# Performance work log

Hardware: AMD Instinct MI355X
Metric: run time of the kernel (lower is better)

## Reference

```python
import jax, jax.numpy as jnp
import numpy as np

TT_IN = (8, 8, 8, 8)
TT_OUT = (8, 8, 8, 8)
TT_RANKS = (1, 32, 32, 32, 1)
BATCH = 4096
N_IN = int(np.prod(TT_IN))     # 4096
N_OUT = int(np.prod(TT_OUT))   # 4096
KERNEL_LEN = int(sum(TT_RANKS[k] * TT_IN[k] * TT_OUT[k] * TT_RANKS[k + 1]
                     for k in range(len(TT_IN))))  # 135168


def setup_inputs() -> dict:
    key = jax.random.key(0)
    kx, kk = jax.random.split(key)
    x = jax.random.normal(kx, (BATCH, N_IN), dtype=jnp.float32)
    # flat packed TT cores (the layer stores all cores in one 1-D weight)
    kernel = 0.02 * jax.random.normal(kk, (KERNEL_LEN,), dtype=jnp.float32)
    bias = jnp.zeros((N_OUT,), dtype=jnp.float32)
    return {"x": x, "kernel": kernel, "bias": bias}


def reference(x, kernel, bias):
    # Faithful translation of TensorTrainDense.call: iterate cores k = d-1 .. 0,
    # slicing the flat kernel from index 0 (matching the original code exactly).
    batch = x.shape[0]
    res = x
    idx = 0
    for k in range(len(TT_IN) - 1, -1, -1):
        m = TT_IN[k] * TT_RANKS[k + 1]   # contraction dim
        n = TT_RANKS[k] * TT_OUT[k]      # output dim of this core
        core = kernel[idx:idx + m * n].reshape(m, n)
        res = res.reshape(-1, m) @ core              # (-1, r_k*out_k)
        res = res.reshape(-1, TT_OUT[k]).T           # (out_k, -1)
        idx += m * n
    res = res.reshape(-1, batch).T                   # (batch, prod(out))
    return res + bias
```

## Files before the change

kernel.cpp:

```cpp
#include <hip/hip_runtime.h>
#include <hip/hip_bf16.h>

typedef unsigned short u16;
typedef __attribute__((ext_vector_type(8))) short  bf16x8;
typedef __attribute__((ext_vector_type(4))) float  fx4;

#define OFF_C0 0
#define OFF_C1 2048
#define OFF_C2 67584
#define OFF_C3 133120

static __device__ __forceinline__ u16 f2bf(float f) {
  union { __hip_bfloat16 h; u16 u; } cv;
  cv.h = __float2bfloat16(f);
  return cv.u;
}
static __device__ __forceinline__ float bf2f(u16 u) {
  union { u16 u; __hip_bfloat16 h; } cv;
  cv.u = u;
  return __bfloat162float(cv.h);
}

__global__ void x_and_w34T(const float* __restrict__ x, u16* __restrict__ xb,
                           const float* __restrict__ ker, float* __restrict__ w34T) {
  if (blockIdx.x < 8192) {
    int t = blockIdx.x * 256 + threadIdx.x;
    const fx4* p = (const fx4*)(x + (size_t)t * 8);
    fx4 v0 = p[0], v1 = p[1];
    u16 tmp[8];
#pragma unroll
    for (int q = 0; q < 4; ++q) tmp[q] = f2bf(v0[q]);
#pragma unroll
    for (int q = 0; q < 4; ++q) tmp[4 + q] = f2bf(v1[q]);
    typedef __attribute__((ext_vector_type(8))) u16 u16x8;
    *(u16x8*)(xb + (size_t)t * 8) = *(const u16x8*)tmp;
  } else {
    int t = (blockIdx.x - 8192) * 256 + threadIdx.x;
    int i34 = t & 63, c = t >> 6;
    int a2 = c >> 6, o3 = (c >> 3) & 7, o4 = c & 7;
    int i3 = i34 >> 3, i4 = i34 & 7;
    float s = 0.f;
#pragma unroll 8
    for (int a3 = 0; a3 < 32; ++a3) {
      float k1 = ker[OFF_C1 + (i3 * 32 + a3) * 256 + a2 * 8 + o3];
      float k0 = ker[OFF_C0 + i4 * 256 + a3 * 8 + o4];
      s += k1 * k0;
    }
    w34T[c * 64 + i34] = s;
  }
}

__global__ void build_w234t2(const float* __restrict__ ker, const float* __restrict__ w34T,
                             u16* __restrict__ w234t) {
  int t = blockIdx.x * 256 + threadIdx.x;
  int i234 = t & 511, g = t >> 9;
  int a1 = g >> 3, o3 = g & 7;
  int i2 = i234 >> 6, i34 = i234 & 63;
  float acc[8][8];
#pragma unroll
  for (int a = 0; a < 8; ++a)
#pragma unroll
    for (int b = 0; b < 8; ++b) acc[a][b] = 0.f;
  for (int a2 = 0; a2 < 32; ++a2) {
    float w[8];
#pragma unroll
    for (int o4 = 0; o4 < 8; ++o4)
      w[o4] = w34T[(a2 * 64 + o3 * 8 + o4) * 64 + i34];
#pragma unroll
    for (int o2 = 0; o2 < 8; ++o2) {
      float c2 = ker[OFF_C2 + (i2 * 32 + a2) * 256 + a1 * 8 + o2];
#pragma unroll
      for (int o4 = 0; o4 < 8; ++o4) acc[o2][o4] += c2 * w[o4];
    }
  }
#pragma unroll
  for (int o2 = 0; o2 < 8; ++o2) {
    int cg = a1 * 64 + o2 * 8 + o3;
#pragma unroll
    for (int o4 = 0; o4 < 8; ++o4)
      w234t[(cg * 8 + o4) * 512 + i234] = f2bf(acc[o2][o4]);
  }
}

__global__ void build_wt2(const float* __restrict__ ker, const u16* __restrict__ w234t,
                          u16* __restrict__ wt) {
  int t = blockIdx.x * 256 + threadIdx.x;
  int i234 = t & 511, j234 = t >> 9;
  float acc[8][8];
#pragma unroll
  for (int a = 0; a < 8; ++a)
#pragma unroll
    for (int b = 0; b < 8; ++b) acc[a][b] = 0.f;
  for (int a1 = 0; a1 < 32; ++a1) {
    float w = bf2f(w234t[(a1 * 512 + j234) * 512 + i234]);
#pragma unroll
    for (int i1 = 0; i1 < 8; ++i1) {
      const float* c3 = ker + OFF_C3 + (i1 * 32 + a1) * 8;
#pragma unroll
      for (int o1 = 0; o1 < 8; ++o1) acc[i1][o1] += c3[o1] * w;
    }
  }
#pragma unroll
  for (int o1 = 0; o1 < 8; ++o1)
#pragma unroll
    for (int i1 = 0; i1 < 8; ++i1)
      wt[(size_t)(o1 * 512 + j234) * 4096 + i1 * 512 + i234] = f2bf(acc[i1][o1]);
}

__device__ __forceinline__ void gld16(const u16* g, u16* l) {
  __builtin_amdgcn_global_load_lds((const __attribute__((address_space(1))) void*)g,
                                   (__attribute__((address_space(3))) void*)l, 16, 0, 0);
}

__global__ __launch_bounds__(256, 2) void gemm_half(const u16* __restrict__ A, const u16* __restrict__ Bt,
                                                    const float* __restrict__ bias, float* __restrict__ C) {
  __shared__ __align__(16) u16 sh[36864];

  const int tid = threadIdx.x;
  const int lane = tid & 63;
  const int wave = tid >> 6;
  const int wm = wave >> 1, wn = wave & 1;
  const int fr = lane & 15, fg = lane >> 4;

  const int bid = blockIdx.x;
  const int wg = (bid & 7) * 64 + (bid >> 3);
  const int bm = (wg >> 4) * 128, bn = (wg & 15) * 256;

  const int lq = lane >> 2, ls = lane & 3;
  size_t agA[2], agB[4];
#pragma unroll
  for (int L = 0; L < 2; ++L) {
    const int row = (wave * 2 + L) * 16 + lq;
    agA[L] = (size_t)(bm + row) * 4096 + ((ls ^ ((row >> 1) & 3)) * 8);
  }
#pragma unroll
  for (int L = 0; L < 4; ++L) {
    const int row = (wave * 4 + L) * 16 + lq;
    agB[L] = (size_t)(bn + row) * 4096 + ((ls ^ ((row >> 1) & 3)) * 8);
  }
  u16* const ldA0 = sh + (wave * 2) * 512;
  u16* const ldB0 = sh + 12288 + (wave * 4) * 512;

  int aoff[4], boff[8];
#pragma unroll
  for (int m = 0; m < 4; ++m) {
    const int R = wm * 64 + m * 16 + fr;
    aoff[m] = R * 32 + ((fg ^ ((R >> 1) & 3)) * 8);
  }
#pragma unroll
  for (int n = 0; n < 8; ++n) {
    const int R = wn * 128 + n * 16 + fr;
    boff[n] = R * 32 + ((fg ^ ((R >> 1) & 3)) * 8);
  }

  fx4 acc[4][8];
#pragma unroll
  for (int m = 0; m < 4; ++m)
#pragma unroll
    for (int n = 0; n < 8; ++n) acc[m][n] = (fx4){0.f, 0.f, 0.f, 0.f};

#define STAGE(buf, t) do { const size_t k_ = (size_t)(((t) & 127) * 32); \
    u16* a_ = ldA0 + (buf) * 4096; u16* b_ = ldB0 + (buf) * 8192; \
    gld16(A + agA[0] + k_, a_); \
    gld16(A + agA[1] + k_, a_ + 512); \
    gld16(Bt + agB[0] + k_, b_); \
    gld16(Bt + agB[1] + k_, b_ + 512); \
    gld16(Bt + agB[2] + k_, b_ + 1024); \
    gld16(Bt + agB[3] + k_, b_ + 1536); } while (0)

  STAGE(0, 0);
  STAGE(1, 1);
  asm volatile("s_waitcnt vmcnt(6)" ::: "memory");
  __builtin_amdgcn_s_barrier();

  int p = 0;
  for (int t = 0; t < 128; ++t) {
    const int ps = p + 2 >= 3 ? p - 1 : p + 2;
    const u16* Ap = sh + p * 4096;
    const u16* Bp = sh + 12288 + p * 8192;

    bf16x8 av[4], bv[8];
#pragma unroll
    for (int m = 0; m < 4; ++m) av[m] = *(const bf16x8*)(Ap + aoff[m]);
#pragma unroll
    for (int n = 0; n < 8; ++n) bv[n] = *(const bf16x8*)(Bp + boff[n]);

    STAGE(ps, t + 2);

    __builtin_amdgcn_s_setprio(1);
#pragma unroll
    for (int m = 0; m < 4; ++m)
#pragma unroll
      for (int n = 0; n < 8; ++n)
        acc[m][n] = __builtin_amdgcn_mfma_f32_16x16x32_bf16(av[m], bv[n], acc[m][n], 0, 0, 0);
    __builtin_amdgcn_s_setprio(0);

    asm volatile("s_waitcnt vmcnt(6)" ::: "memory");
    __builtin_amdgcn_s_barrier();
    p = p + 1 >= 3 ? 0 : p + 1;
  }

  const int crow0 = bm + wm * 64 + fg * 4;
  const int ccol0 = bn + wn * 128 + fr;
#pragma unroll
  for (int n = 0; n < 8; ++n) {
    const int col = ccol0 + n * 16;
    const float bvl = bias[col];
#pragma unroll
    for (int m = 0; m < 4; ++m) {
      const int r0 = crow0 + m * 16;
#pragma unroll
      for (int q = 0; q < 4; ++q)
        C[(size_t)(r0 + q) * 4096 + col] = acc[m][n][q] + bvl;
    }
  }
#undef STAGE
}

extern "C" void kernel_launch(void* const* d_in, const int* in_sizes, int n_in,
                              void* d_out, int out_size, void* d_ws, size_t ws_size,
                              hipStream_t stream) {
  const float* x    = (const float*)d_in[0];
  const float* ker  = (const float*)d_in[1];
  const float* bias = (const float*)d_in[2];
  float* out = (float*)d_out;

  char* ws = (char*)d_ws;
  u16*  xb    = (u16*)ws;
  u16*  wt    = (u16*)(ws + 33554432);
  u16*  w234t = (u16*)(ws + 67108864);
  float* w34T = (float*)(ws + 83886080);

  x_and_w34T  <<<8704, 256, 0, stream>>>(x, xb, ker, w34T);
  build_w234t2<<<512, 256, 0, stream>>>(ker, w34T, w234t);
  build_wt2   <<<1024, 256, 0, stream>>>(ker, w234t, wt);
  gemm_half   <<<512, 256, 0, stream>>>(xb, wt, bias, out);
}
```

Baseline: 211.2 us.

## Pre-pack operands in MFMA fragment layout and use 32x32x16 MFMA with 256x256 tiles

The bf16 conversion of x and the dense weight build now write their outputs directly in a fragment-major layout that matches the 32x32x16 MFMA operand order, so each wave can load its fragments with contiguous 16-byte LDS reads and no swizzle. The GEMM moves from 128x256 tiles with 16x16x32 MFMA to 256x256 tiles with 32x32x16 MFMA, which doubles reuse per tile and halves the grid to 256 blocks at occupancy 1. The aim is to cut LDS traffic and instruction overhead per FLOP. In exchange the GEMM keeps more accumulator registers per thread, has less latency hiding at one block per CU, and the input conversion now reads x with strided row accesses.

```diff
diff --git a/kernel.cpp b/kernel.cpp
--- a/kernel.cpp
+++ b/kernel.cpp
@@ -3,13 +3,16 @@
 
 typedef unsigned short u16;
 typedef __attribute__((ext_vector_type(8))) short  bf16x8;
+typedef __attribute__((ext_vector_type(8))) u16    u16x8;
 typedef __attribute__((ext_vector_type(4))) float  fx4;
+typedef __attribute__((ext_vector_type(16))) float fx16;
 
 #define OFF_C0 0
 #define OFF_C1 2048
 #define OFF_C2 67584
 #define OFF_C3 133120
 
+
 static __device__ __forceinline__ u16 f2bf(float f) {
   union { __hip_bfloat16 h; u16 u; } cv;
   cv.h = __float2bfloat16(f);
@@ -21,19 +24,21 @@
   return __bfloat162float(cv.h);
 }
 
-__global__ void x_and_w34T(const float* __restrict__ x, u16* __restrict__ xb,
+__global__ void x_and_w34T(const float* __restrict__ x, u16* __restrict__ xbt,
                            const float* __restrict__ ker, float* __restrict__ w34T) {
   if (blockIdx.x < 8192) {
     int t = blockIdx.x * 256 + threadIdx.x;
-    const fx4* p = (const fx4*)(x + (size_t)t * 8);
+    int l = t & 63, ks = (t >> 6) & 1, m32 = (t >> 7) & 127, k32 = t >> 14;
+    int row = m32 * 32 + (l & 31);
+    int col = k32 * 32 + ks * 16 + (l >> 5) * 8;
+    const fx4* p = (const fx4*)(x + (size_t)row * 4096 + col);
     fx4 v0 = p[0], v1 = p[1];
     u16 tmp[8];
 #pragma unroll
     for (int q = 0; q < 4; ++q) tmp[q] = f2bf(v0[q]);
 #pragma unroll
     for (int q = 0; q < 4; ++q) tmp[4 + q] = f2bf(v1[q]);
-    typedef __attribute__((ext_vector_type(8))) u16 u16x8;
-    *(u16x8*)(xb + (size_t)t * 8) = *(const u16x8*)tmp;
+    *(u16x8*)(xbt + (size_t)t * 8) = *(const u16x8*)tmp;
   } else {
     int t = (blockIdx.x - 8192) * 256 + threadIdx.x;
     int i34 = t & 63, c = t >> 6;
@@ -82,8 +87,8 @@
   }
 }
 
-__global__ void build_wt2(const float* __restrict__ ker, const u16* __restrict__ w234t,
-                          u16* __restrict__ wt) {
+__global__ void build_wt3(const float* __restrict__ ker, const u16* __restrict__ w234t,
+                          u16* __restrict__ wtt) {
   int t = blockIdx.x * 256 + threadIdx.x;
   int i234 = t & 511, j234 = t >> 9;
   float acc[8][8];
@@ -100,11 +105,18 @@
       for (int o1 = 0; o1 < 8; ++o1) acc[i1][o1] += c3[o1] * w;
     }
   }
-#pragma unroll
-  for (int o1 = 0; o1 < 8; ++o1)
-#pragma unroll
-    for (int i1 = 0; i1 < 8; ++i1)
-      wt[(size_t)(o1 * 512 + j234) * 4096 + i1 * 512 + i234] = f2bf(acc[i1][o1]);
+  const int ks = (i234 >> 4) & 1;
+  const int l  = (j234 & 31) | (((i234 >> 3) & 1) << 5);
+  const int e  = i234 & 7;
+#pragma unroll
+  for (int o1 = 0; o1 < 8; ++o1) {
+    const int n32 = o1 * 16 + (j234 >> 5);
+#pragma unroll
+    for (int i1 = 0; i1 < 8; ++i1) {
+      const int k32 = i1 * 16 + (i234 >> 5);
+      wtt[(((size_t)(k32 * 128 + n32) * 2 + ks) * 64 + l) * 8 + e] = f2bf(acc[i1][o1]);
+    }
+  }
 }
 
 __device__ __forceinline__ void gld16(const u16* g, u16* l) {
@@ -112,78 +124,70 @@
                                    (__attribute__((address_space(3))) void*)l, 16, 0, 0);
 }
 
-__global__ __launch_bounds__(256, 2) void gemm_half(const u16* __restrict__ A, const u16* __restrict__ Bt,
-                                                    const float* __restrict__ bias, float* __restrict__ C) {
-  __shared__ __align__(16) u16 sh[36864];
+__global__ __launch_bounds__(256, 1) void gemm_fm(const u16* __restrict__ A, const u16* __restrict__ B,
+                                                  const float* __restrict__ bias, float* __restrict__ C) {
+  __shared__ __align__(16) u16 sh[49152];
 
   const int tid = threadIdx.x;
   const int lane = tid & 63;
   const int wave = tid >> 6;
   const int wm = wave >> 1, wn = wave & 1;
-  const int fr = lane & 15, fg = lane >> 4;
+  const int l32 = lane & 31, hk = lane >> 5;
 
   const int bid = blockIdx.x;
-  const int wg = (bid & 7) * 64 + (bid >> 3);
-  const int bm = (wg >> 4) * 128, bn = (wg & 15) * 256;
-
-  const int lq = lane >> 2, ls = lane & 3;
-  size_t agA[2], agB[4];
-#pragma unroll
-  for (int L = 0; L < 2; ++L) {
-    const int row = (wave * 2 + L) * 16 + lq;
-    agA[L] = (size_t)(bm + row) * 4096 + ((ls ^ ((row >> 1) & 3)) * 8);
-  }
-#pragma unroll
-  for (int L = 0; L < 4; ++L) {
-    const int row = (wave * 4 + L) * 16 + lq;
-    agB[L] = (size_t)(bn + row) * 4096 + ((ls ^ ((row >> 1) & 3)) * 8);
-  }
-  u16* const ldA0 = sh + (wave * 2) * 512;
-  u16* const ldB0 = sh + 12288 + (wave * 4) * 512;
-
-  int aoff[4], boff[8];
-#pragma unroll
-  for (int m = 0; m < 4; ++m) {
-    const int R = wm * 64 + m * 16 + fr;
-    aoff[m] = R * 32 + ((fg ^ ((R >> 1) & 3)) * 8);
-  }
-#pragma unroll
-  for (int n = 0; n < 8; ++n) {
-    const int R = wn * 128 + n * 16 + fr;
-    boff[n] = R * 32 + ((fg ^ ((R >> 1) & 3)) * 8);
-  }
-
-  fx4 acc[4][8];
+  const int wg = (bid & 7) * 32 + (bid >> 3);
+  const int bm = (wg >> 4) * 256, bn = (wg & 15) * 256;
+
+  size_t agA[4], agB[4];
+#pragma unroll
+  for (int j = 0; j < 4; ++j) {
+    const int u = wave * 4 + j, mf = u >> 1, ks = u & 1;
+    agA[j] = ((size_t)((bm >> 5) + mf) * 2 + ks) * 512 + lane * 8;
+    agB[j] = ((size_t)((bn >> 5) + mf) * 2 + ks) * 512 + lane * 8;
+  }
+  const int ldsU = wave * 4 * 512;
+
+  fx16 acc[4][4];
 #pragma unroll
   for (int m = 0; m < 4; ++m)
 #pragma unroll
-    for (int n = 0; n < 8; ++n) acc[m][n] = (fx4){0.f, 0.f, 0.f, 0.f};
-
-#define STAGE(buf, t) do { const size_t k_ = (size_t)(((t) & 127) * 32); \
-    u16* a_ = ldA0 + (buf) * 4096; u16* b_ = ldB0 + (buf) * 8192; \
-    gld16(A + agA[0] + k_, a_); \
-    gld16(A + agA[1] + k_, a_ + 512); \
-    gld16(Bt + agB[0] + k_, b_); \
-    gld16(Bt + agB[1] + k_, b_ + 512); \
-    gld16(Bt + agB[2] + k_, b_ + 1024); \
-    gld16(Bt + agB[3] + k_, b_ + 1536); } while (0)
+    for (int n = 0; n < 4; ++n)
+#pragma unroll
+      for (int q = 0; q < 16; ++q) acc[m][n][q] = 0.f;
+
+#define STAGE(buf, tt) do { const size_t ko = (size_t)((tt) & 127) * 131072; \
+    u16* a_ = sh + (buf) * 8192 + ldsU; u16* b_ = sh + 24576 + (buf) * 8192 + ldsU; \
+    gld16(A + agA[0] + ko, a_); \
+    gld16(A + agA[1] + ko, a_ + 512); \
+    gld16(A + agA[2] + ko, a_ + 1024); \
+    gld16(A + agA[3] + ko, a_ + 1536); \
+    gld16(B + agB[0] + ko, b_); \
+    gld16(B + agB[1] + ko, b_ + 512); \
+    gld16(B + agB[2] + ko, b_ + 1024); \
+    gld16(B + agB[3] + ko, b_ + 1536); } while (0)
 
   STAGE(0, 0);
   STAGE(1, 1);
-  asm volatile("s_waitcnt vmcnt(6)" ::: "memory");
+  asm volatile("s_waitcnt vmcnt(8)" ::: "memory");
   __builtin_amdgcn_s_barrier();
 
   int p = 0;
   for (int t = 0; t < 128; ++t) {
     const int ps = p + 2 >= 3 ? p - 1 : p + 2;
-    const u16* Ap = sh + p * 4096;
-    const u16* Bp = sh + 12288 + p * 8192;
-
-    bf16x8 av[4], bv[8];
-#pragma unroll
-    for (int m = 0; m < 4; ++m) av[m] = *(const bf16x8*)(Ap + aoff[m]);
-#pragma unroll
-    for (int n = 0; n < 8; ++n) bv[n] = *(const bf16x8*)(Bp + boff[n]);
+    const u16* Ap = sh + p * 8192;
+    const u16* Bp = sh + 24576 + p * 8192;
+
+    bf16x8 a0[4], b0[4], a1[4], b1[4];
+#pragma unroll
+    for (int m = 0; m < 4; ++m) {
+      a0[m] = *(const bf16x8*)(Ap + (wm * 8 + m * 2) * 512 + lane * 8);
+      a1[m] = *(const bf16x8*)(Ap + (wm * 8 + m * 2 + 1) * 512 + lane * 8);
+    }
+#pragma unroll
+    for (int n = 0; n < 4; ++n) {
+      b0[n] = *(const bf16x8*)(Bp + (wn * 8 + n * 2) * 512 + lane * 8);
+      b1[n] = *(const bf16x8*)(Bp + (wn * 8 + n * 2 + 1) * 512 + lane * 8);
+    }
 
     STAGE(ps, t + 2);
 
@@ -191,27 +195,32 @@
 #pragma unroll
     for (int m = 0; m < 4; ++m)
 #pragma unroll
-      for (int n = 0; n < 8; ++n)
-        acc[m][n] = __builtin_amdgcn_mfma_f32_16x16x32_bf16(av[m], bv[n], acc[m][n], 0, 0, 0);
+      for (int n = 0; n < 4; ++n)
+        acc[m][n] = __builtin_amdgcn_mfma_f32_32x32x16_bf16(a0[m], b0[n], acc[m][n], 0, 0, 0);
+#pragma unroll
+    for (int m = 0; m < 4; ++m)
+#pragma unroll
+      for (int n = 0; n < 4; ++n)
+        acc[m][n] = __builtin_amdgcn_mfma_f32_32x32x16_bf16(a1[m], b1[n], acc[m][n], 0, 0, 0);
     __builtin_amdgcn_s_setprio(0);
 
-    asm volatile("s_waitcnt vmcnt(6)" ::: "memory");
+    asm volatile("s_waitcnt vmcnt(8)" ::: "memory");
     __builtin_amdgcn_s_barrier();
     p = p + 1 >= 3 ? 0 : p + 1;
   }
 
-  const int crow0 = bm + wm * 64 + fg * 4;
-  const int ccol0 = bn + wn * 128 + fr;
-#pragma unroll
-  for (int n = 0; n < 8; ++n) {
-    const int col = ccol0 + n * 16;
+#pragma unroll
+  for (int n = 0; n < 4; ++n) {
+    const int col = bn + wn * 128 + n * 32 + l32;
     const float bvl = bias[col];
 #pragma unroll
     for (int m = 0; m < 4; ++m) {
-      const int r0 = crow0 + m * 16;
-#pragma unroll
-      for (int q = 0; q < 4; ++q)
-        C[(size_t)(r0 + q) * 4096 + col] = acc[m][n][q] + bvl;
+      const int r0 = bm + wm * 128 + m * 32 + 4 * hk;
+#pragma unroll
+      for (int q = 0; q < 16; ++q) {
+        const int row = r0 + (q & 3) + 8 * (q >> 2);
+        C[(size_t)row * 4096 + col] = acc[m][n][q] + bvl;
+      }
     }
   }
 #undef STAGE
@@ -226,13 +235,13 @@
   float* out = (float*)d_out;
 
   char* ws = (char*)d_ws;
-  u16*  xb    = (u16*)ws;
-  u16*  wt    = (u16*)(ws + 33554432);
+  u16*  xbt   = (u16*)ws;
+  u16*  wtt   = (u16*)(ws + 33554432);
   u16*  w234t = (u16*)(ws + 67108864);
   float* w34T = (float*)(ws + 83886080);
 
-  x_and_w34T  <<<8704, 256, 0, stream>>>(x, xb, ker, w34T);
+  x_and_w34T  <<<8704, 256, 0, stream>>>(x, xbt, ker, w34T);
   build_w234t2<<<512, 256, 0, stream>>>(ker, w34T, w234t);
-  build_wt2   <<<1024, 256, 0, stream>>>(ker, w234t, wt);
-  gemm_half   <<<512, 256, 0, stream>>>(xb, wt, bias, out);
-}
+  build_wt3   <<<1024, 256, 0, stream>>>(ker, w234t, wtt);
+  gemm_fm     <<<256, 256, 0, stream>>>(xbt, wtt, bias, out);
+}
```

Result: slower. 379.5 us (+79.7%).
